# Kernel optimization log

Measured on AMD Instinct MI355X. Metric: run time of the kernel, lower is better.

Reference implementation:

```python
import jax, jax.numpy as jnp
import numpy as np

D_MODEL = 1024
N_HEADS = 16
DK = D_MODEL // N_HEADS


def setup_inputs() -> dict:
    key = jax.random.key(0)
    ks = jax.random.split(key, 9)
    B, T = 4, 2048
    s = 1.0 / np.sqrt(D_MODEL)
    inp = {
        "x": jax.random.normal(ks[0], (B, T, D_MODEL), dtype=jnp.float32),
        "Wq": jax.random.normal(ks[1], (D_MODEL, D_MODEL), dtype=jnp.float32) * s,
        "bq": jnp.zeros((D_MODEL,), dtype=jnp.float32),
        "Wk": jax.random.normal(ks[2], (D_MODEL, D_MODEL), dtype=jnp.float32) * s,
        "bk": jnp.zeros((D_MODEL,), dtype=jnp.float32),
        "Wv": jax.random.normal(ks[3], (D_MODEL, D_MODEL), dtype=jnp.float32) * s,
        "bv": jnp.zeros((D_MODEL,), dtype=jnp.float32),
        "Wo": jax.random.normal(ks[4], (D_MODEL, D_MODEL), dtype=jnp.float32) * s,
        "bo": jnp.zeros((D_MODEL,), dtype=jnp.float32),
    }
    return inp


def reference(x, Wq, bq, Wk, bk, Wv, bv, Wo, bo):
    B, T, D = x.shape
    H, dk = N_HEADS, DK
    scale = 1.0 / np.sqrt(dk).astype(np.float32)

    def heads(t):  # [B,T,D] -> [B,H,T,dk]
        return t.reshape(B, T, H, dk).transpose(0, 2, 1, 3)

    Q = heads(x @ Wq + bq)
    K = heads(x @ Wk + bk)
    V = heads(x @ Wv + bv)
    scores = jnp.einsum("bhqd,bhkd->bhqk", Q, K) * scale
    attn = jax.nn.softmax(scores, axis=-1)  # dropout inactive at eval
    ctx = jnp.einsum("bhqk,bhkd->bhqd", attn, V)
    ctx = ctx.transpose(0, 2, 1, 3).reshape(B, T, D)
    return ctx @ Wo + bo
```

## Files before the change

kernel.cpp:

```cpp
#include <hip/hip_runtime.h>
#include <hip/hip_bf16.h>
#include <stdint.h>

#define D_MODEL 1024
#define NHEADS  16
#define DK      64
#define TSEQ    2048
#define BATCH   4
#define MROWS   8192

typedef __attribute__((ext_vector_type(8))) short bf16x8;
typedef __attribute__((ext_vector_type(4))) float f32x4;
typedef __attribute__((ext_vector_type(16))) float f32x16;

__device__ __forceinline__ void gl_lds16(const void* g, void* l) {
  __builtin_amdgcn_global_load_lds(
      (const __attribute__((address_space(1))) unsigned int*)g,
      (__attribute__((address_space(3))) unsigned int*)l,
      16, 0, 0);
}

__device__ __forceinline__ short f2bs(float f) {
  union { __hip_bfloat16 h; short s; } u;
  u.h = __float2bfloat16(f);
  return u.s;
}

__device__ __forceinline__ uint32_t cvt_pk(float lo, float hi) {
  uint32_t r;
  asm("s_nop 1\n\tv_cvt_pk_bf16_f32 %0, %1, %2" : "=v"(r) : "v"(lo), "v"(hi));
  return r;
}

__device__ __forceinline__ void permswap(uint32_t& a, uint32_t& b) {
  asm("v_permlane32_swap_b32 %0, %1" : "+v"(a), "+v"(b));
}

__global__ void prep_kernel(
    const float* __restrict__ x, short* __restrict__ xb,
    const float* __restrict__ s0, const float* __restrict__ s1,
    const float* __restrict__ s2, const float* __restrict__ s3,
    short* __restrict__ d0, short* __restrict__ d1,
    short* __restrict__ d2, short* __restrict__ d3) {
  const int z = blockIdx.z;
  if (z < 4) {
    const float* src = (z == 0) ? s0 : (z == 1) ? s1 : (z == 2) ? s2 : s3;
    short* dst = (z == 0) ? d0 : (z == 1) ? d1 : (z == 2) ? d2 : d3;
    __shared__ float tile[32][33];
    const int tx = threadIdx.x, ty = threadIdx.y;
    const int n0 = blockIdx.x * 32, k0 = blockIdx.y * 32;
#pragma unroll
    for (int r = 0; r < 32; r += 8)
      tile[ty + r][tx] = src[(size_t)(k0 + ty + r) * D_MODEL + n0 + tx];
    __syncthreads();
#pragma unroll
    for (int r = 0; r < 32; r += 8)
      dst[(size_t)(n0 + ty + r) * D_MODEL + k0 + tx] = f2bs(tile[tx][ty + r]);
  } else {
    const int c = (z - 4) * 1024 + blockIdx.y * 32 + blockIdx.x;
    const int base = (c * 256 + (int)(threadIdx.y * 32 + threadIdx.x)) * 2;
#pragma unroll
    for (int q = 0; q < 2; ++q) {
      const int i = base + q;
      const float4 v = reinterpret_cast<const float4*>(x)[i];
      short4 r;
      r.x = f2bs(v.x); r.y = f2bs(v.y); r.z = f2bs(v.z); r.w = f2bs(v.w);
      reinterpret_cast<short4*>(xb)[i] = r;
    }
  }
}

#define GEMM_MAIN_LOOP(A_, BT_)                                                     \
  __shared__ short SM[2][16384];              \
  const int tid = threadIdx.x;                                                      \
  const int lane = tid & 63;                                                        \
  const int w = tid >> 6;                                                           \
  const int wm = w >> 1, wn = w & 1;                                                \
  const int rowBase = blockIdx.x * 128;                                             \
  const int colBase = blockIdx.y * 128;                                             \
  const int g = lane >> 4;                                                          \
  const int c15 = lane & 15;                                                        \
  f32x4 acc[4][4];                                                                  \
  _Pragma("unroll")                                                                 \
  for (int i = 0; i < 4; ++i)                                                       \
    _Pragma("unroll")                                                               \
    for (int j = 0; j < 4; ++j) acc[i][j] = {0.f, 0.f, 0.f, 0.f};                   \
  const int srow = lane >> 3;                                                       \
  const int schunk8 = ((lane & 7) ^ srow) * 8;                                      \
  const short* gA = (A_) + (size_t)(rowBase + w * 32 + srow) * 1024 + schunk8;      \
  const short* gB = (BT_) + (size_t)(colBase + w * 32 + srow) * 1024 + schunk8;     \
  const int ko0 = ((g) ^ (c15 & 7)) * 8;                                            \
  const int ko1 = ((4 + g) ^ (c15 & 7)) * 8;                                        \
  _Pragma("unroll")                                                                 \
  for (int c = 0; c < 4; ++c) {                                                     \
    gl_lds16(gA + (size_t)(c * 8) * 1024, &SM[0][(w * 32 + c * 8) * 64]);           \
    gl_lds16(gB + (size_t)(c * 8) * 1024, &SM[0][8192 + (w * 32 + c * 8) * 64]);    \
  }                                                                                 \
  _Pragma("unroll 2")                                                               \
  for (int kt = 0; kt < 1024; kt += 64) {                                           \
    const int buf = (kt >> 6) & 1;                                                  \
    asm volatile("s_waitcnt vmcnt(0)" ::: "memory");                                \
    __builtin_amdgcn_s_barrier();                                                   \
    __builtin_amdgcn_sched_barrier(0);                                              \
    if (kt + 64 < 1024) {                                                           \
      _Pragma("unroll")                                                             \
      for (int c = 0; c < 4; ++c) {                                                 \
        gl_lds16(gA + (size_t)(c * 8) * 1024 + kt + 64, &SM[buf ^ 1][(w * 32 + c * 8) * 64]); \
        gl_lds16(gB + (size_t)(c * 8) * 1024 + kt + 64, &SM[buf ^ 1][8192 + (w * 32 + c * 8) * 64]); \
      }                                                                             \
    }                                                                               \
    const short* smA = &SM[buf][0];                                                 \
    const short* smB = &SM[buf][8192];                                              \
    bf16x8 af[4][2], bfr[4][2];                                                     \
    _Pragma("unroll")                                                               \
    for (int i = 0; i < 4; ++i) {                                                   \
      const int rb = (wm * 64 + i * 16 + c15) * 64;                                 \
      af[i][0] = *reinterpret_cast<const bf16x8*>(&smA[rb + ko0]);                  \
      af[i][1] = *reinterpret_cast<const bf16x8*>(&smA[rb + ko1]);                  \
    }                                                                               \
    _Pragma("unroll")                                                               \
    for (int j = 0; j < 4; ++j) {                                                   \
      const int rb = (wn * 64 + j * 16 + c15) * 64;                                 \
      bfr[j][0] = *reinterpret_cast<const bf16x8*>(&smB[rb + ko0]);                 \
      bfr[j][1] = *reinterpret_cast<const bf16x8*>(&smB[rb + ko1]);                 \
    }                                                                               \
    __builtin_amdgcn_s_setprio(1);                                                  \
    _Pragma("unroll")                                                               \
    for (int kk = 0; kk < 2; ++kk)                                                  \
      _Pragma("unroll")                                                             \
      for (int i = 0; i < 4; ++i)                                                   \
        _Pragma("unroll")                                                           \
        for (int j = 0; j < 4; ++j)                                                 \
          acc[i][j] = __builtin_amdgcn_mfma_f32_16x16x32_bf16(af[i][kk], bfr[j][kk], acc[i][j], 0, 0, 0); \
    __builtin_amdgcn_s_setprio(0);                                                  \
  }                                                                                 \
  __syncthreads();

__global__ __launch_bounds__(256, 2) void gemm_qkv_kernel(
    const short* __restrict__ A, const short* __restrict__ BTm,
    const float* __restrict__ bq, const float* __restrict__ bk,
    const float* __restrict__ bv, short* __restrict__ Qb,
    short* __restrict__ Kb, short* __restrict__ Vtb, float CL) {
  GEMM_MAIN_LOOP(A, BTm)
  const int mat = colBase >> 10;
  if (mat == 2) {
    short* smf = &SM[0][0];
    const int d_base = wn * 64 + c15;
#pragma unroll
    for (int j = 0; j < 4; ++j) {
      const int dl = d_base + j * 16;
      const int gcol = (colBase & 1023) + dl;
      const float bb = bv[gcol];
      const int sw = (dl & 15) << 3;
#pragma unroll
      for (int i = 0; i < 4; ++i) {
        const int tb = wm * 64 + i * 16 + g * 4;
#pragma unroll
        for (int r = 0; r < 4; r += 2) {
          const uint32_t p = cvt_pk(acc[i][j][r] + bb, acc[i][j][r + 1] + bb);
          *reinterpret_cast<uint32_t*>(&smf[dl * 128 + ((tb + r) ^ sw)]) = p;
        }
      }
    }
    __syncthreads();
    const int b0 = rowBase >> 11, t0 = rowBase & 2047;
    const int vcolBase = colBase & 1023;
#pragma unroll
    for (int k = 0; k < 8; ++k) {
      const int cid = k * 256 + tid;
      const int d = cid >> 4;
      const int c = cid & 15;
      const bf16x8 vv = *reinterpret_cast<const bf16x8*>(
          &smf[d * 128 + ((c * 8) ^ ((d & 15) << 3))]);
      *reinterpret_cast<bf16x8*>(
          &Vtb[((size_t)(b0 * 1024 + vcolBase + d)) * 2048 + t0 + c * 8]) = vv;
    }
  } else {
    const float* bp = (mat == 0) ? bq : bk;
    const float scl = (mat == 0) ? CL : 1.0f;
    short* Ob = (mat == 0) ? Qb : Kb;
#pragma unroll
    for (int i = 0; i < 4; ++i) {
#pragma unroll
      for (int j = 0; j < 4; ++j) {
#pragma unroll
        for (int r = 0; r < 4; ++r) {
          const int grow = rowBase + wm * 64 + i * 16 + g * 4 + r;
          const int gcol = (colBase + wn * 64 + j * 16 + c15) & 1023;
          const float v = (acc[i][j][r] + bp[gcol]) * scl;
          const int b = grow >> 11, t = grow & 2047;
          const int h = gcol >> 6, d = gcol & 63;
          Ob[((size_t)(b * NHEADS + h) * TSEQ + t) * DK + d] = f2bs(v);
        }
      }
    }
  }
}

__global__ __launch_bounds__(256, 2) void gemm_out_kernel(
    const short* __restrict__ A, const short* __restrict__ BTm,
    const float* __restrict__ bias, float* __restrict__ Cout) {
  GEMM_MAIN_LOOP(A, BTm)
#pragma unroll
  for (int i = 0; i < 4; ++i) {
#pragma unroll
    for (int j = 0; j < 4; ++j) {
#pragma unroll
      for (int r = 0; r < 4; ++r) {
        const int grow = rowBase + wm * 64 + i * 16 + g * 4 + r;
        const int gcol = colBase + wn * 64 + j * 16 + c15;
        Cout[(size_t)grow * 1024 + gcol] = acc[i][j][r] + bias[gcol];
      }
    }
  }
}

__global__ __launch_bounds__(256, 4) void attn_kernel(
    const short* __restrict__ Qg, const short* __restrict__ Kg,
    const short* __restrict__ Vtg, short* __restrict__ ctx) {
  __shared__ short Ks[2][64 * 64];
  __shared__ short VTs[2][64 * 64];

  const int tid = threadIdx.x;
  const int lane = tid & 63;
  const int w = tid >> 6;
  const int l5 = lane >> 5;
  const int c31 = lane & 31;
  const int lid = blockIdx.x;
  const int bh = (lid >> 7) * 8 + (lid & 7);
  const int qbase = ((lid >> 3) & 15) * 128;
  const int b = bh >> 4, h = bh & 15;

  const short* Qp = Qg + (size_t)bh * TSEQ * DK;
  const short* Kp = Kg + (size_t)bh * TSEQ * DK;
  const short* Vtp = Vtg + (size_t)bh * DK * TSEQ;

  const int qrow = qbase + w * 32 + c31;

  bf16x8 qf[4];
#pragma unroll
  for (int kd = 0; kd < 4; ++kd)
    qf[kd] = *reinterpret_cast<const bf16x8*>(Qp + (size_t)qrow * DK + kd * 16 + l5 * 8);

  f32x16 o0, o1;
#pragma unroll
  for (int r = 0; r < 16; ++r) { o0[r] = 0.f; o1[r] = 0.f; }
  float l_s = 0.f;

  f32x16 z16;
#pragma unroll
  for (int r = 0; r < 16; ++r) z16[r] = 0.f;

  const int srow = w * 8 + (lane >> 3);
  const int soff = ((lane & 7) ^ (lane >> 3) ^ (w & 3)) * 8;
  const int swz = (((c31 & 7) ^ (c31 >> 3)) << 4);

  int offA[4];
#pragma unroll
  for (int kd = 0; kd < 4; ++kd)
    offA[kd] = c31 * 64 + ((((kd * 32 + l5 * 16)) ^ swz) >> 1);

#define STAGE(T, SLOT) do {                                                          \
    const int kt_ = (T) * 64;                                                        \
    _Pragma("unroll")                                                                \
    for (int c = 0; c < 2; ++c) {                                                    \
      const int row_ = c * 32 + srow;                                                \
      gl_lds16(Kp + (size_t)(kt_ + row_) * DK + soff, &Ks[SLOT][(c * 4 + w) * 512]); \
      gl_lds16(Vtp + (size_t)row_ * TSEQ + kt_ + soff, &VTs[SLOT][(c * 4 + w) * 512]); \
    }                                                                                \
  } while (0)

#define BODY(T, SLOT, PREFETCH) do {                                                 \
    asm volatile("s_waitcnt vmcnt(0)" ::: "memory");                                 \
    __builtin_amdgcn_s_barrier();                                                    \
    __builtin_amdgcn_sched_barrier(0);                                               \
    if (PREFETCH) STAGE((T) + 1, (SLOT) ^ 1);                                        \
    const short* ksb = &Ks[SLOT][0];                                                 \
    const short* vtb = &VTs[SLOT][0];                                                \
    __builtin_amdgcn_s_setprio(1);                                                   \
    const bf16x8 kf0a = *reinterpret_cast<const bf16x8*>(ksb + offA[0]);             \
    const bf16x8 kf1a = *reinterpret_cast<const bf16x8*>(ksb + 2048 + offA[0]);      \
    f32x16 s0 = __builtin_amdgcn_mfma_f32_32x32x16_bf16(kf0a, qf[0], z16, 0, 0, 0);  \
    f32x16 s1 = __builtin_amdgcn_mfma_f32_32x32x16_bf16(kf1a, qf[0], z16, 0, 0, 0);  \
    _Pragma("unroll")                                                                \
    for (int kd = 1; kd < 4; ++kd) {                                                 \
      const bf16x8 kf0 = *reinterpret_cast<const bf16x8*>(ksb + offA[kd]);           \
      const bf16x8 kf1 = *reinterpret_cast<const bf16x8*>(ksb + 2048 + offA[kd]);    \
      s0 = __builtin_amdgcn_mfma_f32_32x32x16_bf16(kf0, qf[kd], s0, 0, 0, 0);        \
      s1 = __builtin_amdgcn_mfma_f32_32x32x16_bf16(kf1, qf[kd], s1, 0, 0, 0);        \
    }                                                                                \
    __builtin_amdgcn_s_setprio(0);                                                   \
    float p0 = 0.f, p1 = 0.f, p2 = 0.f, p3 = 0.f;                                    \
    _Pragma("unroll")                                                                \
    for (int r = 0; r < 16; r += 4) {                                                \
      s0[r] = __builtin_amdgcn_exp2f(s0[r]);                                         \
      s0[r + 1] = __builtin_amdgcn_exp2f(s0[r + 1]);                                 \
      s0[r + 2] = __builtin_amdgcn_exp2f(s0[r + 2]);                                 \
      s0[r + 3] = __builtin_amdgcn_exp2f(s0[r + 3]);                                 \
      p0 += s0[r]; p1 += s0[r + 1]; p2 += s0[r + 2]; p3 += s0[r + 3];                \
    }                                                                                \
    _Pragma("unroll")                                                                \
    for (int r = 0; r < 16; r += 4) {                                                \
      s1[r] = __builtin_amdgcn_exp2f(s1[r]);                                         \
      s1[r + 1] = __builtin_amdgcn_exp2f(s1[r + 1]);                                 \
      s1[r + 2] = __builtin_amdgcn_exp2f(s1[r + 2]);                                 \
      s1[r + 3] = __builtin_amdgcn_exp2f(s1[r + 3]);                                 \
      p0 += s1[r]; p1 += s1[r + 1]; p2 += s1[r + 2]; p3 += s1[r + 3];                \
    }                                                                                \
    l_s += (p0 + p1) + (p2 + p3);                                                    \
    uint32_t wa[8], wb[8];                                                           \
    _Pragma("unroll")                                                                \
    for (int t2 = 0; t2 < 8; ++t2) {                                                 \
      wa[t2] = cvt_pk(s0[2 * t2], s0[2 * t2 + 1]);                                   \
      wb[t2] = cvt_pk(s1[2 * t2], s1[2 * t2 + 1]);                                   \
    }                                                                                \
    permswap(wa[0], wa[2]); permswap(wa[1], wa[3]);                                  \
    permswap(wa[4], wa[6]); permswap(wa[5], wa[7]);                                  \
    permswap(wb[0], wb[2]); permswap(wb[1], wb[3]);                                  \
    permswap(wb[4], wb[6]); permswap(wb[5], wb[7]);                                  \
    bf16x8 pf[4];                                                                    \
    {                                                                                \
      union { uint32_t u[4]; bf16x8 v; } fr;                                         \
      fr.u[0] = wa[0]; fr.u[1] = wa[1]; fr.u[2] = wa[2]; fr.u[3] = wa[3]; pf[0] = fr.v; \
      fr.u[0] = wa[4]; fr.u[1] = wa[5]; fr.u[2] = wa[6]; fr.u[3] = wa[7]; pf[1] = fr.v; \
      fr.u[0] = wb[0]; fr.u[1] = wb[1]; fr.u[2] = wb[2]; fr.u[3] = wb[3]; pf[2] = fr.v; \
      fr.u[0] = wb[4]; fr.u[1] = wb[5]; fr.u[2] = wb[6]; fr.u[3] = wb[7]; pf[3] = fr.v; \
    }                                                                                \
    __builtin_amdgcn_s_setprio(1);                                                   \
    _Pragma("unroll")                                                                \
    for (int ks = 0; ks < 4; ++ks) {                                                 \
      const bf16x8 vf0 = *reinterpret_cast<const bf16x8*>(vtb + offA[ks]);           \
      const bf16x8 vf1 = *reinterpret_cast<const bf16x8*>(vtb + 2048 + offA[ks]);    \
      o0 = __builtin_amdgcn_mfma_f32_32x32x16_bf16(vf0, pf[ks], o0, 0, 0, 0);        \
      o1 = __builtin_amdgcn_mfma_f32_32x32x16_bf16(vf1, pf[ks], o1, 0, 0, 0);        \
    }                                                                                \
    __builtin_amdgcn_s_setprio(0);                                                   \
  } while (0)

  STAGE(0, 0);
  for (int t = 0; t < 30; t += 2) {
    BODY(t, 0, true);
    BODY(t + 1, 1, true);
  }
  BODY(30, 0, true);
  BODY(31, 1, false);

#undef STAGE
#undef BODY

  l_s += __shfl_xor(l_s, 32, 64);

  const float inv = 1.0f / l_s;
  short* crow = ctx + ((size_t)b * TSEQ + qrow) * D_MODEL + h * 64;
#pragma unroll
  for (int r = 0; r < 16; r += 2) {
    const int d = (r & 3) + 8 * (r >> 2) + 4 * l5;
    *reinterpret_cast<uint32_t*>(&crow[d]) = cvt_pk(o0[r] * inv, o0[r + 1] * inv);
    *reinterpret_cast<uint32_t*>(&crow[32 + d]) = cvt_pk(o1[r] * inv, o1[r + 1] * inv);
  }
}

extern "C" void kernel_launch(void* const* d_in, const int* in_sizes, int n_in,
                              void* d_out, int out_size, void* d_ws, size_t ws_size,
                              hipStream_t stream) {
  const float* x  = (const float*)d_in[0];
  const float* Wq = (const float*)d_in[1];
  const float* bq = (const float*)d_in[2];
  const float* Wk = (const float*)d_in[3];
  const float* bk = (const float*)d_in[4];
  const float* Wv = (const float*)d_in[5];
  const float* bv = (const float*)d_in[6];
  const float* Wo = (const float*)d_in[7];
  const float* bo = (const float*)d_in[8];
  float* out = (float*)d_out;

  short* xb   = (short*)d_ws;
  short* WqT  = xb + (size_t)MROWS * D_MODEL;
  short* WkT  = WqT + (size_t)D_MODEL * D_MODEL;
  short* WvT  = WkT + (size_t)D_MODEL * D_MODEL;
  short* WoT  = WvT + (size_t)D_MODEL * D_MODEL;
  short* Qb   = WoT + (size_t)D_MODEL * D_MODEL;
  short* Kb   = Qb + (size_t)MROWS * D_MODEL;
  short* Vtb  = Kb + (size_t)MROWS * D_MODEL;
  short* ctxb = xb;

  const float CL = 0.1803368801111204f;

  prep_kernel<<<dim3(32, 32, 8), dim3(32, 8), 0, stream>>>(
      x, xb, Wq, Wk, Wv, Wo, WqT, WkT, WvT, WoT);

  gemm_qkv_kernel<<<dim3(MROWS / 128, 3 * D_MODEL / 128), 256, 0, stream>>>(
      xb, WqT, bq, bk, bv, Qb, Kb, Vtb, CL);

  attn_kernel<<<1024, 256, 0, stream>>>(Qb, Kb, Vtb, ctxb);

  gemm_out_kernel<<<dim3(MROWS / 128, D_MODEL / 128), 256, 0, stream>>>(ctxb, WoT, bo, out);
}
```

Measured before the change: 164.9 us.

## Fuse fp32-to-bf16 conversion of x into QKV GEMM A-tile loading

The QKV GEMM now reads x directly in fp32 through registers, converts it to bf16 and stores it into swizzled LDS, overlapping the loads with the MFMA loop. This removes the separate x-conversion pass and the bf16 x workspace round-trip from the prep kernel. In exchange, A traffic across the column blocks doubles in bytes, more registers are used, and ctx gets its own workspace buffer. The packed-convert helper also drops its leading s_nop.

```diff
diff --git a/kernel.cpp b/kernel.cpp
--- a/kernel.cpp
+++ b/kernel.cpp
@@ -32,42 +32,34 @@
   return r;
 }
 
+__device__ __forceinline__ uint32_t cvt_pk_nh(float lo, float hi) {
+  uint32_t r;
+  asm("v_cvt_pk_bf16_f32 %0, %1, %2" : "=v"(r) : "v"(lo), "v"(hi));
+  return r;
+}
+
 __device__ __forceinline__ void permswap(uint32_t& a, uint32_t& b) {
   asm("v_permlane32_swap_b32 %0, %1" : "+v"(a), "+v"(b));
 }
 
 __global__ void prep_kernel(
-    const float* __restrict__ x, short* __restrict__ xb,
     const float* __restrict__ s0, const float* __restrict__ s1,
     const float* __restrict__ s2, const float* __restrict__ s3,
     short* __restrict__ d0, short* __restrict__ d1,
     short* __restrict__ d2, short* __restrict__ d3) {
   const int z = blockIdx.z;
-  if (z < 4) {
-    const float* src = (z == 0) ? s0 : (z == 1) ? s1 : (z == 2) ? s2 : s3;
-    short* dst = (z == 0) ? d0 : (z == 1) ? d1 : (z == 2) ? d2 : d3;
-    __shared__ float tile[32][33];
-    const int tx = threadIdx.x, ty = threadIdx.y;
-    const int n0 = blockIdx.x * 32, k0 = blockIdx.y * 32;
-#pragma unroll
-    for (int r = 0; r < 32; r += 8)
-      tile[ty + r][tx] = src[(size_t)(k0 + ty + r) * D_MODEL + n0 + tx];
-    __syncthreads();
-#pragma unroll
-    for (int r = 0; r < 32; r += 8)
-      dst[(size_t)(n0 + ty + r) * D_MODEL + k0 + tx] = f2bs(tile[tx][ty + r]);
-  } else {
-    const int c = (z - 4) * 1024 + blockIdx.y * 32 + blockIdx.x;
-    const int base = (c * 256 + (int)(threadIdx.y * 32 + threadIdx.x)) * 2;
-#pragma unroll
-    for (int q = 0; q < 2; ++q) {
-      const int i = base + q;
-      const float4 v = reinterpret_cast<const float4*>(x)[i];
-      short4 r;
-      r.x = f2bs(v.x); r.y = f2bs(v.y); r.z = f2bs(v.z); r.w = f2bs(v.w);
-      reinterpret_cast<short4*>(xb)[i] = r;
-    }
-  }
+  const float* src = (z == 0) ? s0 : (z == 1) ? s1 : (z == 2) ? s2 : s3;
+  short* dst = (z == 0) ? d0 : (z == 1) ? d1 : (z == 2) ? d2 : d3;
+  __shared__ float tile[32][33];
+  const int tx = threadIdx.x, ty = threadIdx.y;
+  const int n0 = blockIdx.x * 32, k0 = blockIdx.y * 32;
+#pragma unroll
+  for (int r = 0; r < 32; r += 8)
+    tile[ty + r][tx] = src[(size_t)(k0 + ty + r) * D_MODEL + n0 + tx];
+  __syncthreads();
+#pragma unroll
+  for (int r = 0; r < 32; r += 8)
+    dst[(size_t)(n0 + ty + r) * D_MODEL + k0 + tx] = f2bs(tile[tx][ty + r]);
 }
 
 #define GEMM_MAIN_LOOP(A_, BT_)                                                     \
@@ -137,11 +129,102 @@
   __syncthreads();
 
 __global__ __launch_bounds__(256, 2) void gemm_qkv_kernel(
-    const short* __restrict__ A, const short* __restrict__ BTm,
+    const float* __restrict__ Af, const short* __restrict__ BTm,
     const float* __restrict__ bq, const float* __restrict__ bk,
     const float* __restrict__ bv, short* __restrict__ Qb,
     short* __restrict__ Kb, short* __restrict__ Vtb, float CL) {
-  GEMM_MAIN_LOOP(A, BTm)
+  __shared__ short SM[2][16384];
+  const int tid = threadIdx.x;
+  const int lane = tid & 63;
+  const int w = tid >> 6;
+  const int wm = w >> 1, wn = w & 1;
+  const int rowBase = blockIdx.x * 128;
+  const int colBase = blockIdx.y * 128;
+  const int g = lane >> 4;
+  const int c15 = lane & 15;
+  f32x4 acc[4][4];
+#pragma unroll
+  for (int i = 0; i < 4; ++i)
+#pragma unroll
+    for (int j = 0; j < 4; ++j) acc[i][j] = {0.f, 0.f, 0.f, 0.f};
+
+  const int sr = lane >> 3;
+  const int lc = lane & 7;
+  const int schunk8 = (lc ^ sr) * 8;
+  const float* gAf = Af + (size_t)(rowBase + w * 32 + sr) * 1024 + lc * 8;
+  const short* gB = BTm + (size_t)(colBase + w * 32 + sr) * 1024 + schunk8;
+  const int ko0 = ((g) ^ (c15 & 7)) * 8;
+  const int ko1 = ((4 + g) ^ (c15 & 7)) * 8;
+
+  f32x4 a0[4], a1[4];
+#define LOADA(KT) do { _Pragma("unroll")                                        \
+    for (int c = 0; c < 4; ++c) {                                               \
+      a0[c] = *reinterpret_cast<const f32x4*>(gAf + (size_t)(c * 8) * 1024 + (KT));     \
+      a1[c] = *reinterpret_cast<const f32x4*>(gAf + (size_t)(c * 8) * 1024 + (KT) + 4); \
+    } } while (0)
+#define LOADB(KT, D) do { _Pragma("unroll")                                     \
+    for (int c = 0; c < 4; ++c)                                                 \
+      gl_lds16(gB + (size_t)(c * 8) * 1024 + (KT), &SM[D][8192 + (w * 32 + c * 8) * 64]); \
+    } while (0)
+#define WRITEA(D) do { _Pragma("unroll")                                        \
+    for (int c = 0; c < 4; ++c) {                                               \
+      union { uint32_t u[4]; bf16x8 v; } fr;                                    \
+      fr.u[0] = cvt_pk_nh(a0[c][0], a0[c][1]);                                  \
+      fr.u[1] = cvt_pk_nh(a0[c][2], a0[c][3]);                                  \
+      fr.u[2] = cvt_pk_nh(a1[c][0], a1[c][1]);                                  \
+      fr.u[3] = cvt_pk_nh(a1[c][2], a1[c][3]);                                  \
+      *reinterpret_cast<bf16x8*>(&SM[D][(w * 32 + c * 8 + sr) * 64 + (lc ^ sr) * 8]) = fr.v; \
+    } } while (0)
+
+  LOADA(0);
+  LOADB(0, 0);
+  asm volatile("s_waitcnt vmcnt(0)" ::: "memory");
+  WRITEA(0);
+
+#pragma unroll 2
+  for (int kt = 0; kt < 1024; kt += 64) {
+    const int buf = (kt >> 6) & 1;
+    asm volatile("s_waitcnt lgkmcnt(0)" ::: "memory");
+    __builtin_amdgcn_s_barrier();
+    __builtin_amdgcn_sched_barrier(0);
+    if (kt + 64 < 1024) {
+      LOADA(kt + 64);
+      LOADB(kt + 64, buf ^ 1);
+    }
+    const short* smA = &SM[buf][0];
+    const short* smB = &SM[buf][8192];
+    bf16x8 af[4][2], bfr[4][2];
+#pragma unroll
+    for (int i = 0; i < 4; ++i) {
+      const int rb = (wm * 64 + i * 16 + c15) * 64;
+      af[i][0] = *reinterpret_cast<const bf16x8*>(&smA[rb + ko0]);
+      af[i][1] = *reinterpret_cast<const bf16x8*>(&smA[rb + ko1]);
+    }
+#pragma unroll
+    for (int j = 0; j < 4; ++j) {
+      const int rb = (wn * 64 + j * 16 + c15) * 64;
+      bfr[j][0] = *reinterpret_cast<const bf16x8*>(&smB[rb + ko0]);
+      bfr[j][1] = *reinterpret_cast<const bf16x8*>(&smB[rb + ko1]);
+    }
+    __builtin_amdgcn_s_setprio(1);
+#pragma unroll
+    for (int kk = 0; kk < 2; ++kk)
+#pragma unroll
+      for (int i = 0; i < 4; ++i)
+#pragma unroll
+        for (int j = 0; j < 4; ++j)
+          acc[i][j] = __builtin_amdgcn_mfma_f32_16x16x32_bf16(af[i][kk], bfr[j][kk], acc[i][j], 0, 0, 0);
+    __builtin_amdgcn_s_setprio(0);
+    if (kt + 64 < 1024) {
+      asm volatile("s_waitcnt vmcnt(0)" ::: "memory");
+      WRITEA(buf ^ 1);
+    }
+  }
+  __syncthreads();
+#undef LOADA
+#undef LOADB
+#undef WRITEA
+
   const int mat = colBase >> 10;
   if (mat == 2) {
     short* smf = &SM[0][0];
@@ -157,7 +240,7 @@
         const int tb = wm * 64 + i * 16 + g * 4;
 #pragma unroll
         for (int r = 0; r < 4; r += 2) {
-          const uint32_t p = cvt_pk(acc[i][j][r] + bb, acc[i][j][r + 1] + bb);
+          const uint32_t p = cvt_pk_nh(acc[i][j][r] + bb, acc[i][j][r + 1] + bb);
           *reinterpret_cast<uint32_t*>(&smf[dl * 128 + ((tb + r) ^ sw)]) = p;
         }
       }
@@ -374,23 +457,22 @@
   const float* bo = (const float*)d_in[8];
   float* out = (float*)d_out;
 
-  short* xb   = (short*)d_ws;
-  short* WqT  = xb + (size_t)MROWS * D_MODEL;
+  short* WqT  = (short*)d_ws;
   short* WkT  = WqT + (size_t)D_MODEL * D_MODEL;
   short* WvT  = WkT + (size_t)D_MODEL * D_MODEL;
   short* WoT  = WvT + (size_t)D_MODEL * D_MODEL;
   short* Qb   = WoT + (size_t)D_MODEL * D_MODEL;
   short* Kb   = Qb + (size_t)MROWS * D_MODEL;
   short* Vtb  = Kb + (size_t)MROWS * D_MODEL;
-  short* ctxb = xb;
+  short* ctxb = Vtb + (size_t)MROWS * D_MODEL;
 
   const float CL = 0.1803368801111204f;
 
-  prep_kernel<<<dim3(32, 32, 8), dim3(32, 8), 0, stream>>>(
-      x, xb, Wq, Wk, Wv, Wo, WqT, WkT, WvT, WoT);
+  prep_kernel<<<dim3(32, 32, 4), dim3(32, 8), 0, stream>>>(
+      Wq, Wk, Wv, Wo, WqT, WkT, WvT, WoT);
 
   gemm_qkv_kernel<<<dim3(MROWS / 128, 3 * D_MODEL / 128), 256, 0, stream>>>(
-      xb, WqT, bq, bk, bv, Qb, Kb, Vtb, CL);
+      x, WqT, bq, bk, bv, Qb, Kb, Vtb, CL);
 
   attn_kernel<<<1024, 256, 0, stream>>>(Qb, Kb, Vtb, ctxb);
 
```

New measurement: 174.1 us. 5.6% more time.

## Software-pipeline PV matmul one tile behind QK with triple-buffered V

Applied to the files above, without the earlier changes.

Restructures the attention inner loop so the P·V MFMAs for the previous key tile are issued right after the current tile's QK MFMAs, before the exp/softmax work. The aim is to overlap matrix-core work with the transcendental and packing ALU work. V tiles are now triple-buffered in LDS so the delayed PV read does not race with the prefetch, and a final epilogue handles the last tile. This costs extra LDS and keeps the P fragments live across iterations, which raises register pressure and may reduce occupancy.

```diff
diff --git a/kernel.cpp b/kernel.cpp
--- a/kernel.cpp
+++ b/kernel.cpp
@@ -219,7 +219,7 @@
     const short* __restrict__ Qg, const short* __restrict__ Kg,
     const short* __restrict__ Vtg, short* __restrict__ ctx) {
   __shared__ short Ks[2][64 * 64];
-  __shared__ short VTs[2][64 * 64];
+  __shared__ short VTs[3][64 * 64];
 
   const int tid = threadIdx.x;
   const int lane = tid & 63;
@@ -251,6 +251,8 @@
 #pragma unroll
   for (int r = 0; r < 16; ++r) z16[r] = 0.f;
 
+  bf16x8 pf[4] = {};
+
   const int srow = w * 8 + (lane >> 3);
   const int soff = ((lane & 7) ^ (lane >> 3) ^ (w & 3)) * 8;
   const int swz = (((c31 & 7) ^ (c31 >> 3)) << 4);
@@ -260,23 +262,22 @@
   for (int kd = 0; kd < 4; ++kd)
     offA[kd] = c31 * 64 + ((((kd * 32 + l5 * 16)) ^ swz) >> 1);
 
-#define STAGE(T, SLOT) do {                                                          \
+#define STAGE(T, KSLOT, VSLOT) do {                                                  \
     const int kt_ = (T) * 64;                                                        \
     _Pragma("unroll")                                                                \
     for (int c = 0; c < 2; ++c) {                                                    \
       const int row_ = c * 32 + srow;                                                \
-      gl_lds16(Kp + (size_t)(kt_ + row_) * DK + soff, &Ks[SLOT][(c * 4 + w) * 512]); \
-      gl_lds16(Vtp + (size_t)row_ * TSEQ + kt_ + soff, &VTs[SLOT][(c * 4 + w) * 512]); \
+      gl_lds16(Kp + (size_t)(kt_ + row_) * DK + soff, &Ks[KSLOT][(c * 4 + w) * 512]); \
+      gl_lds16(Vtp + (size_t)row_ * TSEQ + kt_ + soff, &VTs[VSLOT][(c * 4 + w) * 512]); \
     }                                                                                \
   } while (0)
 
-#define BODY(T, SLOT, PREFETCH) do {                                                 \
+#define BODY(T, KS, VSP, VSS, PREFETCH, DO_PV) do {                                  \
     asm volatile("s_waitcnt vmcnt(0)" ::: "memory");                                 \
     __builtin_amdgcn_s_barrier();                                                    \
     __builtin_amdgcn_sched_barrier(0);                                               \
-    if (PREFETCH) STAGE((T) + 1, (SLOT) ^ 1);                                        \
-    const short* ksb = &Ks[SLOT][0];                                                 \
-    const short* vtb = &VTs[SLOT][0];                                                \
+    if (PREFETCH) STAGE((T) + 1, (KS) ^ 1, VSS);                                     \
+    const short* ksb = &Ks[KS][0];                                                   \
     __builtin_amdgcn_s_setprio(1);                                                   \
     const bf16x8 kf0a = *reinterpret_cast<const bf16x8*>(ksb + offA[0]);             \
     const bf16x8 kf1a = *reinterpret_cast<const bf16x8*>(ksb + 2048 + offA[0]);      \
@@ -289,6 +290,16 @@
       s0 = __builtin_amdgcn_mfma_f32_32x32x16_bf16(kf0, qf[kd], s0, 0, 0, 0);        \
       s1 = __builtin_amdgcn_mfma_f32_32x32x16_bf16(kf1, qf[kd], s1, 0, 0, 0);        \
     }                                                                                \
+    if (DO_PV) {                                                                     \
+      const short* vtb = &VTs[VSP][0];                                               \
+      _Pragma("unroll")                                                              \
+      for (int ks = 0; ks < 4; ++ks) {                                               \
+        const bf16x8 vf0 = *reinterpret_cast<const bf16x8*>(vtb + offA[ks]);         \
+        const bf16x8 vf1 = *reinterpret_cast<const bf16x8*>(vtb + 2048 + offA[ks]);  \
+        o0 = __builtin_amdgcn_mfma_f32_32x32x16_bf16(vf0, pf[ks], o0, 0, 0, 0);      \
+        o1 = __builtin_amdgcn_mfma_f32_32x32x16_bf16(vf1, pf[ks], o1, 0, 0, 0);      \
+      }                                                                              \
+    }                                                                                \
     __builtin_amdgcn_s_setprio(0);                                                   \
     float p0 = 0.f, p1 = 0.f, p2 = 0.f, p3 = 0.f;                                    \
     _Pragma("unroll")                                                                \
@@ -318,7 +329,6 @@
     permswap(wa[4], wa[6]); permswap(wa[5], wa[7]);                                  \
     permswap(wb[0], wb[2]); permswap(wb[1], wb[3]);                                  \
     permswap(wb[4], wb[6]); permswap(wb[5], wb[7]);                                  \
-    bf16x8 pf[4];                                                                    \
     {                                                                                \
       union { uint32_t u[4]; bf16x8 v; } fr;                                         \
       fr.u[0] = wa[0]; fr.u[1] = wa[1]; fr.u[2] = wa[2]; fr.u[3] = wa[3]; pf[0] = fr.v; \
@@ -326,24 +336,32 @@
       fr.u[0] = wb[0]; fr.u[1] = wb[1]; fr.u[2] = wb[2]; fr.u[3] = wb[3]; pf[2] = fr.v; \
       fr.u[0] = wb[4]; fr.u[1] = wb[5]; fr.u[2] = wb[6]; fr.u[3] = wb[7]; pf[3] = fr.v; \
     }                                                                                \
-    __builtin_amdgcn_s_setprio(1);                                                   \
-    _Pragma("unroll")                                                                \
-    for (int ks = 0; ks < 4; ++ks) {                                                 \
-      const bf16x8 vf0 = *reinterpret_cast<const bf16x8*>(vtb + offA[ks]);           \
-      const bf16x8 vf1 = *reinterpret_cast<const bf16x8*>(vtb + 2048 + offA[ks]);    \
-      o0 = __builtin_amdgcn_mfma_f32_32x32x16_bf16(vf0, pf[ks], o0, 0, 0, 0);        \
-      o1 = __builtin_amdgcn_mfma_f32_32x32x16_bf16(vf1, pf[ks], o1, 0, 0, 0);        \
-    }                                                                                \
-    __builtin_amdgcn_s_setprio(0);                                                   \
   } while (0)
 
-  STAGE(0, 0);
-  for (int t = 0; t < 30; t += 2) {
-    BODY(t, 0, true);
-    BODY(t + 1, 1, true);
-  }
-  BODY(30, 0, true);
-  BODY(31, 1, false);
+  STAGE(0, 0, 0);
+  for (int t6 = 0; t6 < 30; t6 += 6) {
+    BODY(t6 + 0, 0, 2, 1, true, (t6 > 0));
+    BODY(t6 + 1, 1, 0, 2, true, true);
+    BODY(t6 + 2, 0, 1, 0, true, true);
+    BODY(t6 + 3, 1, 2, 1, true, true);
+    BODY(t6 + 4, 0, 0, 2, true, true);
+    BODY(t6 + 5, 1, 1, 0, true, true);
+  }
+  BODY(30, 0, 2, 1, true, true);
+  BODY(31, 1, 0, 0, false, true);
+
+  {
+    const short* vtb = &VTs[1][0];
+    __builtin_amdgcn_s_setprio(1);
+#pragma unroll
+    for (int ks = 0; ks < 4; ++ks) {
+      const bf16x8 vf0 = *reinterpret_cast<const bf16x8*>(vtb + offA[ks]);
+      const bf16x8 vf1 = *reinterpret_cast<const bf16x8*>(vtb + 2048 + offA[ks]);
+      o0 = __builtin_amdgcn_mfma_f32_32x32x16_bf16(vf0, pf[ks], o0, 0, 0, 0);
+      o1 = __builtin_amdgcn_mfma_f32_32x32x16_bf16(vf1, pf[ks], o1, 0, 0, 0);
+    }
+    __builtin_amdgcn_s_setprio(0);
+  }
 
 #undef STAGE
 #undef BODY
```

Measured after the change: 433.6 us. 2.63x slower.
